# Performance work log

Measured on AMD Instinct MI355X. Metric: run time of the kernel, lower is better.

## Reference

```python
import jax, jax.numpy as jnp
import numpy as np

N = 50000
E = 800000
D = 512
H = 256
K = 16
COLLAPSE_REG = 1.0


def setup_inputs() -> dict:
    key = jax.random.key(0)
    ks = jax.random.split(key, 8)
    embeddings = jax.random.normal(ks[0], (N, D), dtype=jnp.float32)
    edge_src = jax.random.randint(ks[1], (E,), 0, N, dtype=jnp.int32)
    edge_dst = jax.random.randint(ks[2], (E,), 0, N, dtype=jnp.int32)
    # GCNConv params (glorot-ish scaling)
    W1 = jax.random.normal(ks[3], (D, H), dtype=jnp.float32) / np.sqrt(D)
    b1 = jnp.zeros((H,), dtype=jnp.float32)
    W2 = jax.random.normal(ks[4], (H, H), dtype=jnp.float32) / np.sqrt(H)
    b2 = jnp.zeros((H,), dtype=jnp.float32)
    Wa = jax.random.normal(ks[5], (H, K), dtype=jnp.float32) / np.sqrt(H)
    ba = jnp.zeros((K,), dtype=jnp.float32)
    return {"embeddings": embeddings, "edge_src": edge_src, "edge_dst": edge_dst,
            "W1": W1, "b1": b1, "W2": W2, "b2": b2, "Wa": Wa, "ba": ba}


def _gcn_conv(x, W, b, src, dst, dis):
    # PyG GCNConv: transform then D^{-1/2}(A+I)D^{-1/2} aggregation + bias.
    x = x @ W                                   # [N, out]
    norm = dis[src] * dis[dst]                  # [E]
    agg = jax.ops.segment_sum(x[src] * norm[:, None], dst, num_segments=N)
    agg = agg + (dis * dis)[:, None] * x        # self-loop term
    return agg + b


def reference(embeddings, edge_src, edge_dst, W1, b1, W2, b2, Wa, ba):
    # symmetric-norm degrees with self-loops (edge weight 1)
    deg = 1.0 + jax.ops.segment_sum(jnp.ones((E,), jnp.float32), edge_dst, num_segments=N)
    dis = jax.lax.rsqrt(deg)                    # deg > 0 always (self-loop)

    x = jax.nn.selu(_gcn_conv(embeddings, W1, b1, edge_src, edge_dst, dis))
    x_skip = x  # dropout is identity in eval
    x = jax.nn.selu(_gcn_conv(x, W2, b2, edge_src, edge_dst, dis))
    x = x + x_skip
    assignments = jax.nn.softmax(x @ Wa + ba, axis=1)   # [N, K]

    # ---- DMoN losses (faithful to original, incl. scalar normalizer) ----
    degrees = jax.ops.segment_sum(jnp.ones((E,), jnp.float32), edge_src, num_segments=N)  # row sums of A
    m = degrees.sum() / 2.0
    AS = jax.ops.segment_sum(assignments[edge_dst], edge_src, num_segments=N)  # A @ S, [N, K]
    trace_pooled = jnp.sum(assignments * AS)    # trace(S^T A S)
    dS = degrees @ assignments                  # [K]
    normalizer = jnp.dot(dS, dS) / (2.0 * m)    # scalar (as in original code)
    spectral_loss = -(trace_pooled - K * normalizer) / (2.0 * m)

    cluster_sizes = assignments.sum(axis=0)     # [K]
    collapse_loss = jnp.linalg.norm(cluster_sizes) / N * jnp.sqrt(jnp.float32(K)) - 1.0
    entropy = -jnp.sum(assignments * jnp.log(assignments + 1e-8)) / N
    entropy_loss = -0.1 * entropy
    total_loss = spectral_loss + COLLAPSE_REG * collapse_loss + entropy_loss

    pooled = (assignments / (cluster_sizes + 1e-8)).T @ embeddings  # [K, D]
    return (assignments, pooled, spectral_loss, COLLAPSE_REG * collapse_loss, total_loss, entropy_loss)
```

## Files before the change

### kernel.cpp

```cpp
#include <hip/hip_runtime.h>
#include <hip/hip_fp16.h>
#include <math.h>

#define NN 50000
#define EE 800000
#define DD 512
#define HH 256
#define KK 16
#define NB_SCAN 196

typedef _Float16 half8_t __attribute__((ext_vector_type(8)));
typedef float f32x4 __attribute__((ext_vector_type(4)));

__global__ void zero_kernel(int* __restrict__ p, int n) {
    int i = blockIdx.x * blockDim.x + threadIdx.x;
    if (i < n) p[i] = 0;
}

__global__ void count_kernel(const int* __restrict__ src, const int* __restrict__ dst,
                             int* __restrict__ indeg, int* __restrict__ outdeg) {
    int e = blockIdx.x * blockDim.x + threadIdx.x;
    if (e < EE) {
        atomicAdd(&indeg[dst[e]], 1);
        atomicAdd(&outdeg[src[e]], 1);
    }
}

__global__ void node_prep(const int* __restrict__ indeg, const int* __restrict__ outdeg,
                          float* __restrict__ dis, float* __restrict__ degf) {
    int n = blockIdx.x * blockDim.x + threadIdx.x;
    if (n < NN) {
        dis[n]  = 1.0f / sqrtf(1.0f + (float)indeg[n]);
        degf[n] = (float)outdeg[n];
    }
}

__global__ void scan_p1(const int* __restrict__ in, int* __restrict__ part, int n) {
    __shared__ int tile[256];
    int t = threadIdx.x;
    int i = blockIdx.x * 256 + t;
    tile[t] = (i < n) ? in[i] : 0;
    __syncthreads();
    for (int o = 128; o > 0; o >>= 1) {
        if (t < o) tile[t] += tile[t + o];
        __syncthreads();
    }
    if (t == 0) part[blockIdx.x] = tile[0];
}

__global__ void scan_p2(int* __restrict__ part, int nb, int* __restrict__ off_end) {
    __shared__ int tile[256];
    int t = threadIdx.x;
    int v = (t < nb) ? part[t] : 0;
    tile[t] = v;
    __syncthreads();
    for (int o = 1; o < 256; o <<= 1) {
        int x = (t >= o) ? tile[t - o] : 0;
        __syncthreads();
        tile[t] += x;
        __syncthreads();
    }
    if (t < nb) part[t] = tile[t] - v;
    if (t == 255) *off_end = tile[255];
}

__global__ void scan_p3(const int* __restrict__ in, const int* __restrict__ part,
                        int* __restrict__ out, int n) {
    __shared__ int tile[256];
    int t = threadIdx.x;
    int i = blockIdx.x * 256 + t;
    int v = (i < n) ? in[i] : 0;
    tile[t] = v;
    __syncthreads();
    for (int o = 1; o < 256; o <<= 1) {
        int x = (t >= o) ? tile[t - o] : 0;
        __syncthreads();
        tile[t] += x;
        __syncthreads();
    }
    if (i < n) out[i] = part[blockIdx.x] + tile[t] - v;
}

__global__ void scatter_kernel(const int* __restrict__ src, const int* __restrict__ dst,
                               const int* __restrict__ off, int* __restrict__ cur,
                               int* __restrict__ nbr) {
    int e = blockIdx.x * blockDim.x + threadIdx.x;
    if (e < EE) {
        int s = src[e], d = dst[e];
        int p = atomicAdd(&cur[d], 1);
        nbr[off[d] + p] = s;
    }
}

__global__ void transpose_w(const float* __restrict__ W, __half* __restrict__ Wt,
                            int Kdim, int Ndim) {
    int i = blockIdx.x * 256 + threadIdx.x;
    if (i < Kdim * Ndim) {
        int k = i / Ndim, n = i % Ndim;
        Wt[(size_t)n * Kdim + k] = __float2half(W[i]);
    }
}

#define APAD 40

__device__ inline void load16h(const float* p, _Float16* o) {
#pragma unroll
    for (int i = 0; i < 16; i += 4) {
        float4 v = *(const float4*)(p + i);
        o[i] = (_Float16)v.x; o[i + 1] = (_Float16)v.y;
        o[i + 2] = (_Float16)v.z; o[i + 3] = (_Float16)v.w;
    }
}
__device__ inline void load16h(const __half* p, _Float16* o) {
    uint4 v0 = *(const uint4*)p;
    uint4 v1 = *(const uint4*)(p + 8);
    *(uint4*)o = v0;
    *(uint4*)(o + 8) = v1;
}

template <typename TA>
__global__ __launch_bounds__(256) void mfma_gemm(const TA* __restrict__ A,
                                                 const __half* __restrict__ Bt,
                                                 __half* __restrict__ C,
                                                 int M, int Nn, int Kk) {
    __shared__ _Float16 As[128][APAD];
    __shared__ _Float16 Bs[128][APAD];
    int t = threadIdx.x;
    int wave = t >> 6, lane = t & 63;
    int quad = lane >> 4, l16 = lane & 15;
    int row0 = blockIdx.y * 128, col0 = blockIdx.x * 128;
    int wm = (wave & 1) * 64, wn = (wave >> 1) * 64;

    f32x4 acc[4][4] = {};

    int sr = t >> 1;
    int sk = (t & 1) * 16;

    for (int k0 = 0; k0 < Kk; k0 += 32) {
        {
            _Float16 tmp[16];
            int gr = row0 + sr;
            if (gr < M) {
                load16h(A + (size_t)gr * Kk + k0 + sk, tmp);
            } else {
#pragma unroll
                for (int i = 0; i < 16; i++) tmp[i] = (_Float16)0.f;
            }
            *(uint4*)&As[sr][sk] = *(uint4*)tmp;
            *(uint4*)&As[sr][sk + 8] = *(uint4*)(tmp + 8);
        }
        {
            _Float16 tmp[16];
            load16h(Bt + (size_t)(col0 + sr) * Kk + k0 + sk, tmp);
            *(uint4*)&Bs[sr][sk] = *(uint4*)tmp;
            *(uint4*)&Bs[sr][sk + 8] = *(uint4*)(tmp + 8);
        }
        __syncthreads();

        half8_t af[4], bf[4];
#pragma unroll
        for (int mi = 0; mi < 4; mi++)
            af[mi] = *(const half8_t*)&As[wm + mi * 16 + l16][quad * 8];
#pragma unroll
        for (int ni = 0; ni < 4; ni++)
            bf[ni] = *(const half8_t*)&Bs[wn + ni * 16 + l16][quad * 8];
#pragma unroll
        for (int mi = 0; mi < 4; mi++)
#pragma unroll
            for (int ni = 0; ni < 4; ni++)
                acc[mi][ni] = __builtin_amdgcn_mfma_f32_16x16x32_f16(
                    af[mi], bf[ni], acc[mi][ni], 0, 0, 0);
        __syncthreads();
    }

#pragma unroll
    for (int mi = 0; mi < 4; mi++) {
#pragma unroll
        for (int r = 0; r < 4; r++) {
            int rr = row0 + wm + mi * 16 + quad * 4 + r;
            if (rr < M) {
#pragma unroll
                for (int ni = 0; ni < 4; ni++) {
                    C[(size_t)rr * Nn + col0 + wn + ni * 16 + l16] =
                        __float2half(acc[mi][ni][r]);
                }
            }
        }
    }
}

__device__ inline void acc8(float* acc, const __half* p, float w) {
    uint4 raw = *(const uint4*)p;
    const __half2* h = (const __half2*)&raw;
#pragma unroll
    for (int i = 0; i < 4; i++) {
        float2 f = __half22float2(h[i]);
        acc[2 * i]     += w * f.x;
        acc[2 * i + 1] += w * f.y;
    }
}

__global__ __launch_bounds__(256) void agg_selu(const __half* __restrict__ T,
                                                const float* __restrict__ dis,
                                                const int* __restrict__ off,
                                                const int* __restrict__ nbr,
                                                const float* __restrict__ bias,
                                                const __half* skip, __half* out) {
    int t = threadIdx.x;
    int lane = t & 63;
    int l32 = lane & 31;
    int n = blockIdx.x * 8 + (t >> 5);
    int c = l32 * 8;
    float dn = dis[n];

    float acc[8];
    acc8_init: ;
#pragma unroll
    for (int i = 0; i < 8; i++) acc[i] = 0.f;
    acc8(acc, T + (size_t)n * HH + c, dn * dn);

    int s0 = off[n], s1 = off[n + 1];
    int sidv = 0;
    float sdsv = 0.f;
    for (int base = s0; base < s1; base += 32) {
        int cnt = min(32, s1 - base);
        if (l32 < cnt) {
            sidv = nbr[base + l32];
            sdsv = dis[sidv] * dn;
        }
        for (int j = 0; j < cnt; j++) {
            int s = __shfl(sidv, j, 32);
            float w = __shfl(sdsv, j, 32);
            acc8(acc, T + (size_t)s * HH + c, w);
        }
    }

    const float scale = 1.0507009873554805f;
    const float alpha = 1.6732632423543772f;
    float4 b0 = *(const float4*)(bias + c);
    float4 b1 = *(const float4*)(bias + c + 4);
    float bb[8] = {b0.x, b0.y, b0.z, b0.w, b1.x, b1.y, b1.z, b1.w};
    float sk8[8];
#pragma unroll
    for (int i = 0; i < 8; i++) sk8[i] = 0.f;
    if (skip) {
        uint4 raw = *(const uint4*)(skip + (size_t)n * HH + c);
        const __half2* h = (const __half2*)&raw;
#pragma unroll
        for (int i = 0; i < 4; i++) {
            float2 f = __half22float2(h[i]);
            sk8[2 * i] = f.x; sk8[2 * i + 1] = f.y;
        }
    }
    _Float16 res[8];
#pragma unroll
    for (int i = 0; i < 8; i++) {
        float v = acc[i] + bb[i];
        float r = v > 0.f ? scale * v : scale * alpha * expm1f(v);
        res[i] = (_Float16)(r + sk8[i]);
    }
    *(uint4*)(out + (size_t)n * HH + c) = *(uint4*)res;
}

__global__ __launch_bounds__(256) void assign_kernel(const __half* __restrict__ X,
                                                     const float* __restrict__ Wa,
                                                     const float* __restrict__ ba,
                                                     const float* __restrict__ degf,
                                                     float* __restrict__ out_assign,
                                                     float* __restrict__ scal) {
    __shared__ float sWa[HH * KK];
    __shared__ float sX[16][HH];
    __shared__ float scs[KK], sdS[KK], sent_s;
    int t = threadIdx.x;
    int nb = blockIdx.x * 16;
    for (int i = t; i < HH * KK; i += 256) sWa[i] = Wa[i];
    for (int r = 0; r < 16; r++) sX[r][t] = __half2float(X[(size_t)(nb + r) * HH + t]);
    if (t < KK) { scs[t] = 0.f; sdS[t] = 0.f; }
    if (t == 0) sent_s = 0.f;
    __syncthreads();

    int k = t & 15, nl = t >> 4;
    float logit = ba[k];
    for (int c = 0; c < HH; c++) logit += sX[nl][c] * sWa[c * KK + k];

    float mx = logit;
    for (int o = 1; o < 16; o <<= 1) mx = fmaxf(mx, __shfl_xor(mx, o, 16));
    float e = expf(logit - mx);
    float sum = e;
    for (int o = 1; o < 16; o <<= 1) sum += __shfl_xor(sum, o, 16);
    float a = e / sum;
    int node = nb + nl;
    out_assign[(size_t)node * KK + k] = a;

    atomicAdd(&scs[k], a);
    atomicAdd(&sdS[k], degf[node] * a);
    float ent = a * logf(a + 1e-8f);
    for (int o = 32; o >= 1; o >>= 1) ent += __shfl_xor(ent, o);
    if ((t & 63) == 0) atomicAdd(&sent_s, ent);
    __syncthreads();
    if (t < KK) {
        atomicAdd(&scal[t], scs[t]);
        atomicAdd(&scal[16 + t], sdS[t]);
    }
    if (t == 0) atomicAdd(&scal[33], sent_s);
}

__global__ __launch_bounds__(256) void edge_trace(const int* __restrict__ src,
                                                  const int* __restrict__ dst,
                                                  const float* __restrict__ assign,
                                                  float* __restrict__ scal) {
    int e = blockIdx.x * blockDim.x + threadIdx.x;
    float p = 0.f;
    if (e < EE) {
        int s = src[e], d = dst[e];
        const float4* pa = (const float4*)(assign + (size_t)s * KK);
        const float4* pb = (const float4*)(assign + (size_t)d * KK);
#pragma unroll
        for (int i = 0; i < 4; i++) {
            float4 x = pa[i], y = pb[i];
            p += x.x * y.x + x.y * y.y + x.z * y.z + x.w * y.w;
        }
    }
    for (int o = 32; o >= 1; o >>= 1) p += __shfl_xor(p, o);
    __shared__ float sp;
    if (threadIdx.x == 0) sp = 0.f;
    __syncthreads();
    if ((threadIdx.x & 63) == 0) atomicAdd(&sp, p);
    __syncthreads();
    if (threadIdx.x == 0) atomicAdd(&scal[32], sp);
}

#define PCHUNK 250
__global__ __launch_bounds__(256) void pooled_partial(const float* __restrict__ emb,
                                                      const float* __restrict__ assign,
                                                      float* __restrict__ pool_acc) {
    int d = blockIdx.x * 256 + threadIdx.x;
    int c0 = blockIdx.y * PCHUNK;
    float acc[KK];
#pragma unroll
    for (int k = 0; k < KK; k++) acc[k] = 0.f;
    __shared__ float sa[128 * KK];
    for (int sub = 0; sub < PCHUNK; sub += 128) {
        int cnt = min(128, PCHUNK - sub);
        for (int i = threadIdx.x; i < cnt * KK; i += 256)
            sa[i] = assign[(size_t)(c0 + sub) * KK + i];
        __syncthreads();
        for (int j = 0; j < cnt; j++) {
            float ev = emb[(size_t)(c0 + sub + j) * DD + d];
#pragma unroll
            for (int k = 0; k < KK; k++) acc[k] += sa[j * KK + k] * ev;
        }
        __syncthreads();
    }
#pragma unroll
    for (int k = 0; k < KK; k++) atomicAdd(&pool_acc[k * DD + d], acc[k]);
}

__global__ void finalize(const float* __restrict__ pool_acc, const float* __restrict__ scal,
                         float* __restrict__ out) {
    int bx = blockIdx.x, t = threadIdx.x;
    if (bx < 32) {
        int i = bx * 256 + t;
        int k = i / DD;
        out[800000 + i] = pool_acc[i] / (scal[k] + 1e-8f);
    } else if (t == 0) {
        float cs2 = 0.f, ds2 = 0.f;
        for (int k = 0; k < KK; k++) {
            cs2 += scal[k] * scal[k];
            ds2 += scal[16 + k] * scal[16 + k];
        }
        float two_m = (float)EE;
        float normalizer = ds2 / two_m;
        float trace = scal[32];
        float spectral = -(trace - (float)KK * normalizer) / two_m;
        float collapse = sqrtf(cs2) / (float)NN * 4.0f - 1.0f;
        float entl = 0.1f * scal[33] / (float)NN;
        out[808192] = spectral;
        out[808193] = collapse;
        out[808194] = spectral + collapse + entl;
        out[808195] = entl;
    }
}

extern "C" void kernel_launch(void* const* d_in, const int* in_sizes, int n_in,
                              void* d_out, int out_size, void* d_ws, size_t ws_size,
                              hipStream_t stream) {
    const float* emb = (const float*)d_in[0];
    const int* esrc  = (const int*)d_in[1];
    const int* edst  = (const int*)d_in[2];
    const float* W1  = (const float*)d_in[3];
    const float* b1  = (const float*)d_in[4];
    const float* W2  = (const float*)d_in[5];
    const float* b2  = (const float*)d_in[6];
    const float* Wa  = (const float*)d_in[7];
    const float* ba  = (const float*)d_in[8];
    float* out = (float*)d_out;

    int* indeg      = (int*)d_ws;
    int* outdeg     = indeg + 50000;
    int* cur        = outdeg + 50000;
    float* pool_acc = (float*)(cur + 50000);
    float* scal     = pool_acc + 8192;
    int* part       = (int*)(scal + 64);
    int* off        = part + 256;
    int* nbr        = off + 50004;
    float* dis      = (float*)(nbr + 800000);
    float* degf     = dis + 50000;
    __half* Wt1     = (__half*)(degf + 50000);
    __half* Wt2     = Wt1 + 256 * 512;
    __half* T       = Wt2 + 256 * 256;
    __half* Hb      = T + (size_t)NN * HH;

    zero_kernel<<<dim3(619), 256, 0, stream>>>((int*)d_ws, 158256);
    count_kernel<<<dim3(3125), 256, 0, stream>>>(esrc, edst, indeg, outdeg);
    node_prep<<<dim3(196), 256, 0, stream>>>(indeg, outdeg, dis, degf);

    scan_p1<<<dim3(NB_SCAN), 256, 0, stream>>>(indeg, part, NN);
    scan_p2<<<dim3(1), 256, 0, stream>>>(part, NB_SCAN, off + NN);
    scan_p3<<<dim3(NB_SCAN), 256, 0, stream>>>(indeg, part, off, NN);
    scatter_kernel<<<dim3(3125), 256, 0, stream>>>(esrc, edst, off, cur, nbr);

    transpose_w<<<dim3(512), 256, 0, stream>>>(W1, Wt1, DD, HH);
    transpose_w<<<dim3(256), 256, 0, stream>>>(W2, Wt2, HH, HH);

    mfma_gemm<float><<<dim3(2, 391), 256, 0, stream>>>(emb, Wt1, T, NN, HH, DD);
    agg_selu<<<dim3(6250), 256, 0, stream>>>(T, dis, off, nbr, b1, nullptr, Hb);

    mfma_gemm<__half><<<dim3(2, 391), 256, 0, stream>>>(Hb, Wt2, T, NN, HH, HH);
    agg_selu<<<dim3(6250), 256, 0, stream>>>(T, dis, off, nbr, b2, Hb, Hb);

    assign_kernel<<<dim3(3125), 256, 0, stream>>>(Hb, Wa, ba, degf, out, scal);
    edge_trace<<<dim3(3125), 256, 0, stream>>>(esrc, edst, out, scal);
    pooled_partial<<<dim3(2, 200), 256, 0, stream>>>(emb, out, pool_acc);
    finalize<<<dim3(33), 256, 0, stream>>>(pool_acc, scal, out);
}
```

Before: 650.9 us.

## Double-buffer GEMM, vectorize edge kernels, fuse prep kernels, use fp16 assignments

The GEMM is rewritten to double-buffer the A tile in shared memory and prefetch it through registers. The B operand is now read straight from global memory into registers, and the fp32 A tile stays fp32 in LDS and is converted to half when the fragments are read. The count and scatter kernels each handle four edges per thread using int4 loads. node_prep is folded into scan_p1 and the two weight transposes become a single launch. The aggregation kernel unrolls its neighbour gathers by four, and edge_trace reads a half-precision copy of the assignments, which lowers precision in the trace loss.

```diff
diff --git a/kernel.cpp b/kernel.cpp
--- a/kernel.cpp
+++ b/kernel.cpp
@@ -17,29 +17,30 @@
     if (i < n) p[i] = 0;
 }
 
-__global__ void count_kernel(const int* __restrict__ src, const int* __restrict__ dst,
+__global__ void count_kernel(const int4* __restrict__ src4, const int4* __restrict__ dst4,
                              int* __restrict__ indeg, int* __restrict__ outdeg) {
     int e = blockIdx.x * blockDim.x + threadIdx.x;
-    if (e < EE) {
-        atomicAdd(&indeg[dst[e]], 1);
-        atomicAdd(&outdeg[src[e]], 1);
-    }
-}
-
-__global__ void node_prep(const int* __restrict__ indeg, const int* __restrict__ outdeg,
-                          float* __restrict__ dis, float* __restrict__ degf) {
-    int n = blockIdx.x * blockDim.x + threadIdx.x;
-    if (n < NN) {
-        dis[n]  = 1.0f / sqrtf(1.0f + (float)indeg[n]);
-        degf[n] = (float)outdeg[n];
-    }
-}
-
-__global__ void scan_p1(const int* __restrict__ in, int* __restrict__ part, int n) {
+    if (e < EE / 4) {
+        int4 s = src4[e], d = dst4[e];
+        atomicAdd(&outdeg[s.x], 1); atomicAdd(&outdeg[s.y], 1);
+        atomicAdd(&outdeg[s.z], 1); atomicAdd(&outdeg[s.w], 1);
+        atomicAdd(&indeg[d.x], 1);  atomicAdd(&indeg[d.y], 1);
+        atomicAdd(&indeg[d.z], 1);  atomicAdd(&indeg[d.w], 1);
+    }
+}
+
+__global__ void scan_p1(const int* __restrict__ in, int* __restrict__ part, int n,
+                        const int* __restrict__ outdeg, float* __restrict__ dis,
+                        float* __restrict__ degf) {
     __shared__ int tile[256];
     int t = threadIdx.x;
     int i = blockIdx.x * 256 + t;
-    tile[t] = (i < n) ? in[i] : 0;
+    int v = (i < n) ? in[i] : 0;
+    tile[t] = v;
+    if (i < n) {
+        dis[i]  = 1.0f / sqrtf(1.0f + (float)v);
+        degf[i] = (float)outdeg[i];
+    }
     __syncthreads();
     for (int o = 128; o > 0; o >>= 1) {
         if (t < o) tile[t] += tile[t + o];
@@ -81,95 +82,125 @@
     if (i < n) out[i] = part[blockIdx.x] + tile[t] - v;
 }
 
-__global__ void scatter_kernel(const int* __restrict__ src, const int* __restrict__ dst,
+__global__ void scatter_kernel(const int4* __restrict__ src4, const int4* __restrict__ dst4,
                                const int* __restrict__ off, int* __restrict__ cur,
                                int* __restrict__ nbr) {
     int e = blockIdx.x * blockDim.x + threadIdx.x;
-    if (e < EE) {
-        int s = src[e], d = dst[e];
-        int p = atomicAdd(&cur[d], 1);
-        nbr[off[d] + p] = s;
-    }
-}
-
-__global__ void transpose_w(const float* __restrict__ W, __half* __restrict__ Wt,
-                            int Kdim, int Ndim) {
+    if (e < EE / 4) {
+        int4 s = src4[e], d = dst4[e];
+        int p;
+        p = atomicAdd(&cur[d.x], 1); nbr[off[d.x] + p] = s.x;
+        p = atomicAdd(&cur[d.y], 1); nbr[off[d.y] + p] = s.y;
+        p = atomicAdd(&cur[d.z], 1); nbr[off[d.z] + p] = s.z;
+        p = atomicAdd(&cur[d.w], 1); nbr[off[d.w] + p] = s.w;
+    }
+}
+
+__global__ void transpose_w(const float* __restrict__ W1, __half* __restrict__ Wt1,
+                            const float* __restrict__ W2, __half* __restrict__ Wt2) {
     int i = blockIdx.x * 256 + threadIdx.x;
-    if (i < Kdim * Ndim) {
-        int k = i / Ndim, n = i % Ndim;
-        Wt[(size_t)n * Kdim + k] = __float2half(W[i]);
-    }
-}
-
-#define APAD 40
-
-__device__ inline void load16h(const float* p, _Float16* o) {
-#pragma unroll
-    for (int i = 0; i < 16; i += 4) {
-        float4 v = *(const float4*)(p + i);
-        o[i] = (_Float16)v.x; o[i + 1] = (_Float16)v.y;
-        o[i + 2] = (_Float16)v.z; o[i + 3] = (_Float16)v.w;
-    }
-}
-__device__ inline void load16h(const __half* p, _Float16* o) {
-    uint4 v0 = *(const uint4*)p;
-    uint4 v1 = *(const uint4*)(p + 8);
-    *(uint4*)o = v0;
-    *(uint4*)(o + 8) = v1;
-}
-
-template <typename TA>
+    if (i < DD * HH) {
+        int k = i / HH, n = i % HH;
+        Wt1[(size_t)n * DD + k] = __float2half(W1[i]);
+    } else {
+        int j = i - DD * HH;
+        int k = j / HH, n = j % HH;
+        Wt2[(size_t)n * HH + k] = __float2half(W2[j]);
+    }
+}
+
+template <typename TA, int KDIM>
 __global__ __launch_bounds__(256) void mfma_gemm(const TA* __restrict__ A,
                                                  const __half* __restrict__ Bt,
-                                                 __half* __restrict__ C,
-                                                 int M, int Nn, int Kk) {
-    __shared__ _Float16 As[128][APAD];
-    __shared__ _Float16 Bs[128][APAD];
-    int t = threadIdx.x;
-    int wave = t >> 6, lane = t & 63;
-    int quad = lane >> 4, l16 = lane & 15;
-    int row0 = blockIdx.y * 128, col0 = blockIdx.x * 128;
+                                                 __half* __restrict__ C, int M) {
+    constexpr bool F32 = sizeof(TA) == 4;
+    constexpr int SROW = F32 ? 36 : 40;
+    constexpr int EPG  = F32 ? 4 : 8;
+    constexpr int GPR  = 32 / EPG;
+    constexpr int RPP  = 256 / GPR;
+    constexpr int NP   = 128 / RPP;
+    constexpr int KI   = KDIM / 32;
+
+    __shared__ TA As[2][128 * SROW];
+
+    int t = threadIdx.x;
+    int wave = t >> 6, lane = t & 63, quad = lane >> 4, l16 = lane & 15;
+    int row0 = blockIdx.x * 128, col0 = blockIdx.y * 128;
     int wm = (wave & 1) * 64, wn = (wave >> 1) * 64;
+    int srow = t / GPR, sg = t % GPR;
 
     f32x4 acc[4][4] = {};
-
-    int sr = t >> 1;
-    int sk = (t & 1) * 16;
-
-    for (int k0 = 0; k0 < Kk; k0 += 32) {
-        {
-            _Float16 tmp[16];
-            int gr = row0 + sr;
-            if (gr < M) {
-                load16h(A + (size_t)gr * Kk + k0 + sk, tmp);
+    uint4 sreg[NP];
+    uint4 bcur[4];
+
+    const __half* brow[4];
+#pragma unroll
+    for (int ni = 0; ni < 4; ni++)
+        brow[ni] = Bt + (size_t)(col0 + wn + ni * 16 + l16) * KDIM + quad * 8;
+
+    auto gloadA = [&](int k0) {
+#pragma unroll
+        for (int p = 0; p < NP; p++) {
+            int gr = row0 + p * RPP + srow;
+            if (gr < M)
+                sreg[p] = *(const uint4*)(A + (size_t)gr * KDIM + k0 + sg * EPG);
+            else
+                sreg[p] = make_uint4(0, 0, 0, 0);
+        }
+    };
+    auto sstore = [&](int buf) {
+#pragma unroll
+        for (int p = 0; p < NP; p++)
+            *(uint4*)&As[buf][(p * RPP + srow) * SROW + sg * EPG] = sreg[p];
+    };
+
+    gloadA(0);
+#pragma unroll
+    for (int ni = 0; ni < 4; ni++) bcur[ni] = *(const uint4*)(brow[ni]);
+    sstore(0);
+    __syncthreads();
+
+#pragma unroll
+    for (int i = 0; i < KI; i++) {
+        int cur = i & 1;
+        uint4 bnext[4];
+        if (i + 1 < KI) {
+            gloadA((i + 1) * 32);
+#pragma unroll
+            for (int ni = 0; ni < 4; ni++)
+                bnext[ni] = *(const uint4*)(brow[ni] + (i + 1) * 32);
+        }
+
+        half8_t af[4];
+#pragma unroll
+        for (int mi = 0; mi < 4; mi++) {
+            int row = wm + mi * 16 + l16;
+            if constexpr (F32) {
+                const float* pl = (const float*)&As[cur][0] + row * SROW + quad * 8;
+                float4 x0 = *(const float4*)pl;
+                float4 x1 = *(const float4*)(pl + 4);
+                half8_t h;
+                h[0] = (_Float16)x0.x; h[1] = (_Float16)x0.y;
+                h[2] = (_Float16)x0.z; h[3] = (_Float16)x0.w;
+                h[4] = (_Float16)x1.x; h[5] = (_Float16)x1.y;
+                h[6] = (_Float16)x1.z; h[7] = (_Float16)x1.w;
+                af[mi] = h;
             } else {
-#pragma unroll
-                for (int i = 0; i < 16; i++) tmp[i] = (_Float16)0.f;
+                af[mi] = *(const half8_t*)&As[cur][row * SROW + quad * 8];
             }
-            *(uint4*)&As[sr][sk] = *(uint4*)tmp;
-            *(uint4*)&As[sr][sk + 8] = *(uint4*)(tmp + 8);
-        }
-        {
-            _Float16 tmp[16];
-            load16h(Bt + (size_t)(col0 + sr) * Kk + k0 + sk, tmp);
-            *(uint4*)&Bs[sr][sk] = *(uint4*)tmp;
-            *(uint4*)&Bs[sr][sk + 8] = *(uint4*)(tmp + 8);
-        }
-        __syncthreads();
-
-        half8_t af[4], bf[4];
-#pragma unroll
-        for (int mi = 0; mi < 4; mi++)
-            af[mi] = *(const half8_t*)&As[wm + mi * 16 + l16][quad * 8];
-#pragma unroll
-        for (int ni = 0; ni < 4; ni++)
-            bf[ni] = *(const half8_t*)&Bs[wn + ni * 16 + l16][quad * 8];
+        }
 #pragma unroll
         for (int mi = 0; mi < 4; mi++)
 #pragma unroll
             for (int ni = 0; ni < 4; ni++)
                 acc[mi][ni] = __builtin_amdgcn_mfma_f32_16x16x32_f16(
-                    af[mi], bf[ni], acc[mi][ni], 0, 0, 0);
+                    af[mi], *(half8_t*)&bcur[ni], acc[mi][ni], 0, 0, 0);
+
+        if (i + 1 < KI) {
+            sstore(cur ^ 1);
+#pragma unroll
+            for (int ni = 0; ni < 4; ni++) bcur[ni] = bnext[ni];
+        }
         __syncthreads();
     }
 
@@ -181,7 +212,7 @@
             if (rr < M) {
 #pragma unroll
                 for (int ni = 0; ni < 4; ni++) {
-                    C[(size_t)rr * Nn + col0 + wn + ni * 16 + l16] =
+                    C[(size_t)rr * HH + col0 + wn + ni * 16 + l16] =
                         __float2half(acc[mi][ni][r]);
                 }
             }
@@ -189,8 +220,7 @@
     }
 }
 
-__device__ inline void acc8(float* acc, const __half* p, float w) {
-    uint4 raw = *(const uint4*)p;
+__device__ inline void fma8(float* acc, uint4 raw, float w) {
     const __half2* h = (const __half2*)&raw;
 #pragma unroll
     for (int i = 0; i < 4; i++) {
@@ -207,31 +237,41 @@
                                                 const float* __restrict__ bias,
                                                 const __half* skip, __half* out) {
     int t = threadIdx.x;
-    int lane = t & 63;
-    int l32 = lane & 31;
+    int l32 = t & 31;
     int n = blockIdx.x * 8 + (t >> 5);
     int c = l32 * 8;
     float dn = dis[n];
 
     float acc[8];
-    acc8_init: ;
 #pragma unroll
     for (int i = 0; i < 8; i++) acc[i] = 0.f;
-    acc8(acc, T + (size_t)n * HH + c, dn * dn);
+    fma8(acc, *(const uint4*)(T + (size_t)n * HH + c), dn * dn);
 
     int s0 = off[n], s1 = off[n + 1];
-    int sidv = 0;
-    float sdsv = 0.f;
     for (int base = s0; base < s1; base += 32) {
         int cnt = min(32, s1 - base);
+        int sidv = 0; float sdsv = 0.f;
         if (l32 < cnt) {
             sidv = nbr[base + l32];
             sdsv = dis[sidv] * dn;
         }
-        for (int j = 0; j < cnt; j++) {
+        int j = 0;
+        for (; j + 4 <= cnt; j += 4) {
+            int a0 = __shfl(sidv, j, 32),     a1 = __shfl(sidv, j + 1, 32);
+            int a2 = __shfl(sidv, j + 2, 32), a3 = __shfl(sidv, j + 3, 32);
+            float w0 = __shfl(sdsv, j, 32),     w1 = __shfl(sdsv, j + 1, 32);
+            float w2 = __shfl(sdsv, j + 2, 32), w3 = __shfl(sdsv, j + 3, 32);
+            uint4 r0 = *(const uint4*)(T + (size_t)a0 * HH + c);
+            uint4 r1 = *(const uint4*)(T + (size_t)a1 * HH + c);
+            uint4 r2 = *(const uint4*)(T + (size_t)a2 * HH + c);
+            uint4 r3 = *(const uint4*)(T + (size_t)a3 * HH + c);
+            fma8(acc, r0, w0); fma8(acc, r1, w1);
+            fma8(acc, r2, w2); fma8(acc, r3, w3);
+        }
+        for (; j < cnt; j++) {
             int s = __shfl(sidv, j, 32);
             float w = __shfl(sdsv, j, 32);
-            acc8(acc, T + (size_t)s * HH + c, w);
+            fma8(acc, *(const uint4*)(T + (size_t)s * HH + c), w);
         }
     }
 
@@ -267,6 +307,7 @@
                                                      const float* __restrict__ ba,
                                                      const float* __restrict__ degf,
                                                      float* __restrict__ out_assign,
+                                                     __half* __restrict__ out_f16,
                                                      float* __restrict__ scal) {
     __shared__ float sWa[HH * KK];
     __shared__ float sX[16][HH];
@@ -291,6 +332,7 @@
     float a = e / sum;
     int node = nb + nl;
     out_assign[(size_t)node * KK + k] = a;
+    out_f16[(size_t)node * KK + k] = __float2half(a);
 
     atomicAdd(&scs[k], a);
     atomicAdd(&sdS[k], degf[node] * a);
@@ -307,18 +349,28 @@
 
 __global__ __launch_bounds__(256) void edge_trace(const int* __restrict__ src,
                                                   const int* __restrict__ dst,
-                                                  const float* __restrict__ assign,
+                                                  const __half* __restrict__ Ah,
                                                   float* __restrict__ scal) {
     int e = blockIdx.x * blockDim.x + threadIdx.x;
     float p = 0.f;
     if (e < EE) {
         int s = src[e], d = dst[e];
-        const float4* pa = (const float4*)(assign + (size_t)s * KK);
-        const float4* pb = (const float4*)(assign + (size_t)d * KK);
+        uint4 sa = *(const uint4*)(Ah + (size_t)s * KK);
+        uint4 sb = *(const uint4*)(Ah + (size_t)s * KK + 8);
+        uint4 da = *(const uint4*)(Ah + (size_t)d * KK);
+        uint4 db = *(const uint4*)(Ah + (size_t)d * KK + 8);
+        const __half2* xs = (const __half2*)&sa;
+        const __half2* xd = (const __half2*)&da;
 #pragma unroll
         for (int i = 0; i < 4; i++) {
-            float4 x = pa[i], y = pb[i];
-            p += x.x * y.x + x.y * y.y + x.z * y.z + x.w * y.w;
+            float2 u = __half22float2(xs[i]), v = __half22float2(xd[i]);
+            p += u.x * v.x + u.y * v.y;
+        }
+        xs = (const __half2*)&sb; xd = (const __half2*)&db;
+#pragma unroll
+        for (int i = 0; i < 4; i++) {
+            float2 u = __half22float2(xs[i]), v = __half22float2(xd[i]);
+            p += u.x * v.x + u.y * v.y;
         }
     }
     for (int o = 32; o >= 1; o >>= 1) p += __shfl_xor(p, o);
@@ -410,27 +462,28 @@
     __half* Wt2     = Wt1 + 256 * 512;
     __half* T       = Wt2 + 256 * 256;
     __half* Hb      = T + (size_t)NN * HH;
+    __half* Ah      = T;
 
     zero_kernel<<<dim3(619), 256, 0, stream>>>((int*)d_ws, 158256);
-    count_kernel<<<dim3(3125), 256, 0, stream>>>(esrc, edst, indeg, outdeg);
-    node_prep<<<dim3(196), 256, 0, stream>>>(indeg, outdeg, dis, degf);
-
-    scan_p1<<<dim3(NB_SCAN), 256, 0, stream>>>(indeg, part, NN);
+    count_kernel<<<dim3(782), 256, 0, stream>>>((const int4*)esrc, (const int4*)edst,
+                                                indeg, outdeg);
+
+    scan_p1<<<dim3(NB_SCAN), 256, 0, stream>>>(indeg, part, NN, outdeg, dis, degf);
     scan_p2<<<dim3(1), 256, 0, stream>>>(part, NB_SCAN, off + NN);
     scan_p3<<<dim3(NB_SCAN), 256, 0, stream>>>(indeg, part, off, NN);
-    scatter_kernel<<<dim3(3125), 256, 0, stream>>>(esrc, edst, off, cur, nbr);
-
-    transpose_w<<<dim3(512), 256, 0, stream>>>(W1, Wt1, DD, HH);
-    transpose_w<<<dim3(256), 256, 0, stream>>>(W2, Wt2, HH, HH);
-
-    mfma_gemm<float><<<dim3(2, 391), 256, 0, stream>>>(emb, Wt1, T, NN, HH, DD);
+    scatter_kernel<<<dim3(782), 256, 0, stream>>>((const int4*)esrc, (const int4*)edst,
+                                                  off, cur, nbr);
+
+    transpose_w<<<dim3(768), 256, 0, stream>>>(W1, Wt1, W2, Wt2);
+
+    mfma_gemm<float, DD><<<dim3(392, 2), 256, 0, stream>>>(emb, Wt1, T, NN);
     agg_selu<<<dim3(6250), 256, 0, stream>>>(T, dis, off, nbr, b1, nullptr, Hb);
 
-    mfma_gemm<__half><<<dim3(2, 391), 256, 0, stream>>>(Hb, Wt2, T, NN, HH, HH);
+    mfma_gemm<__half, HH><<<dim3(392, 2), 256, 0, stream>>>(Hb, Wt2, T, NN);
     agg_selu<<<dim3(6250), 256, 0, stream>>>(T, dis, off, nbr, b2, Hb, Hb);
 
-    assign_kernel<<<dim3(3125), 256, 0, stream>>>(Hb, Wa, ba, degf, out, scal);
-    edge_trace<<<dim3(3125), 256, 0, stream>>>(esrc, edst, out, scal);
+    assign_kernel<<<dim3(3125), 256, 0, stream>>>(Hb, Wa, ba, degf, out, Ah, scal);
+    edge_trace<<<dim3(3125), 256, 0, stream>>>(esrc, edst, Ah, scal);
     pooled_partial<<<dim3(2, 200), 256, 0, stream>>>(emb, out, pool_acc);
     finalize<<<dim3(33), 256, 0, stream>>>(pool_acc, scal, out);
 }
```

After: 642.3 us. About the same (-1.3%).
